# Optimization experiments

Measured on AMD Instinct MI355X. Metric: run time of the kernel, lower is better.

The kernel has to match this reference:

```python
import jax, jax.numpy as jnp
import numpy as np

N_HEAD = 16
HEAD_DIM = 64


def _shift(BD):
    # BD: [b, n, L, 2L] -> [b, n, L, L] (Transformer-XL left-shift trick)
    b, n, L, _ = BD.shape
    BD = jnp.pad(BD, ((0, 0), (0, 0), (0, 0), (0, 1)))          # [b,n,L,2L+1]
    BD = BD.reshape(b, n, 2 * L + 1, L)[:, :, :-1]              # [b,n,2L,L]
    BD = BD.reshape(b, n, L, 2 * L)[:, :, :, L:]                # [b,n,L,L]
    return BD


def _transpose_shift(E):
    # E: [b, n, L, 2L] -> [b, n, L, L]
    b, n, L, _ = E.shape
    E = jnp.pad(E, ((0, 0), (0, 0), (0, 0), (0, 1)))            # [b,n,L,2L+1]
    E = E.reshape(b, n, 2 * L + 1, L)                           # [b,n,2L+1,L]
    E = E[:, :, 1::2, :]                                        # rows 1,3,...,2L-1 -> [b,n,L,L]
    return E


def setup_inputs() -> dict:
    key = jax.random.key(0)
    ks = jax.random.split(key, 6)
    B, L, D = 4, 1024, 1024
    return {
        "x": jax.random.normal(ks[0], (B, L, D), jnp.float32),
        "pos_embed": jax.random.normal(ks[1], (2 * L, HEAD_DIM), jnp.float32),
        "W_qkv": jax.random.normal(ks[2], (D, 3 * D), jnp.float32) * (1.0 / np.sqrt(D)),
        "b_qkv": jax.random.normal(ks[3], (3 * D,), jnp.float32) * 0.01,
        "r_r_bias": jax.random.normal(ks[4], (N_HEAD, HEAD_DIM), jnp.float32) * 0.02,
        "r_w_bias": jax.random.normal(ks[5], (N_HEAD, HEAD_DIM), jnp.float32) * 0.02,
    }


def reference(x, pos_embed, W_qkv, b_qkv, r_r_bias, r_w_bias):
    b, L, d_model = x.shape
    scale = jnp.sqrt(jnp.asarray(HEAD_DIM, x.dtype))

    qkv = x @ W_qkv + b_qkv                                      # [b,L,3D]
    q, k, v = jnp.split(qkv, 3, axis=-1)

    def split_heads(t):  # [b,L,D] -> [b,n,L,hd]
        return t.reshape(b, L, N_HEAD, HEAD_DIM).transpose(0, 2, 1, 3)

    q, k, v = split_heads(q), split_heads(k), split_heads(v)

    rw_head_q = q + r_r_bias[None, :, None, :]
    AC = jnp.einsum('bnqd,bnkd->bnqk', rw_head_q, k)             # [b,n,L,L]
    D_ = jnp.einsum('nd,ld->nl', r_w_bias, pos_embed)[None, :, None, :]  # [1,n,1,2L]
    B_ = jnp.einsum('bnqd,ld->bnql', q, pos_embed)               # [b,n,L,2L]
    E_ = jnp.einsum('bnqd,ld->bnql', k, pos_embed)               # [b,n,L,2L]

    BDE = _shift(B_ + D_) + _transpose_shift(E_)
    attn = jax.nn.softmax((AC + BDE) / scale, axis=-1)

    out = jnp.einsum('bnqk,bnkd->bnqd', attn, v)                 # [b,n,L,hd]
    out = out.transpose(0, 2, 1, 3).reshape(b, L, d_model)       # merge heads
    return out
```

## Files before the change

### kernel.cpp

```cpp
#include <hip/hip_runtime.h>
#include <math.h>

typedef unsigned short u16;
typedef unsigned int u32;
typedef __attribute__((ext_vector_type(8))) short bf16x8;
typedef __attribute__((ext_vector_type(4))) float f32x4;

#define AS1 __attribute__((address_space(1)))
#define AS3 __attribute__((address_space(3)))

static __device__ __forceinline__ u16 f2b(float f) {
  u32 u = __float_as_uint(f);
  return (u16)((u + 0x7FFFu + ((u >> 16) & 1u)) >> 16);
}
static __device__ __forceinline__ float b2f(u16 b) {
  return __uint_as_float(((u32)b) << 16);
}

__global__ __launch_bounds__(256) void prep(
    const float* __restrict__ x, const float* __restrict__ W,
    const float* __restrict__ P,
    u16* __restrict__ xb, u16* __restrict__ Wt, u16* __restrict__ Pb)
{
  __shared__ u16 sT[64 * 68];
  const int bid = blockIdx.x, t = threadIdx.x;
  if (bid < 4096) {
    const size_t base = (size_t)bid * 1024 + t * 4;
    const float4 v = *(const float4*)(x + base);
    const u32 lo = (u32)f2b(v.x) | ((u32)f2b(v.y) << 16);
    const u32 hi = (u32)f2b(v.z) | ((u32)f2b(v.w) << 16);
    *(uint2*)(xb + base) = make_uint2(lo, hi);
  } else if (bid < 4224) {
    const size_t base = (size_t)(bid - 4096) * 1024 + t * 4;
    const float4 v = *(const float4*)(P + base);
    const u32 lo = (u32)f2b(v.x) | ((u32)f2b(v.y) << 16);
    const u32 hi = (u32)f2b(v.z) | ((u32)f2b(v.w) << 16);
    *(uint2*)(Pb + base) = make_uint2(lo, hi);
  } else if (bid < 4992) {
    const int tb = bid - 4224;
    const int tk = tb / 48, tn = tb % 48;
    const int k0 = tk * 64, n0 = tn * 64;
#pragma unroll
    for (int it = 0; it < 4; ++it) {
      const int c = it * 256 + t;
      const int r = c >> 4, c4 = (c & 15) << 2;
      const float4 v = *(const float4*)(W + (size_t)(k0 + r) * 3072 + n0 + c4);
      sT[(c4 + 0) * 68 + r] = f2b(v.x);
      sT[(c4 + 1) * 68 + r] = f2b(v.y);
      sT[(c4 + 2) * 68 + r] = f2b(v.z);
      sT[(c4 + 3) * 68 + r] = f2b(v.w);
    }
    __syncthreads();
#pragma unroll
    for (int it = 0; it < 4; ++it) {
      const int c = it * 256 + t;
      const int rr = c >> 4, k4 = (c & 15) << 2;
      const uint2 rv = *(const uint2*)(sT + rr * 68 + k4);
      *(uint2*)(Wt + (size_t)(n0 + rr) * 1024 + k0 + k4) = rv;
    }
  } else {
    if (t < 64) Pb[2048 * 64 + t] = f2b(P[2047 * 64 + t]);
  }
}

__global__ __launch_bounds__(256, 3) void qkv_gemm(
    const u16* __restrict__ xb, const u16* __restrict__ Wt,
    const float* __restrict__ bq,
    u16* __restrict__ Qh, u16* __restrict__ Kh, u16* __restrict__ Vt)
{
  __shared__ u16 smem[16384];
  u16* const sA = smem;
  u16* const sB = smem + 8192;
  u16* const T  = smem;
  const int t = threadIdx.x;
  const int lane = t & 63, w = t >> 6;
  const int l = lane & 15, ql = lane >> 4;
  const int wm = w & 1, wn = w >> 1;
  const int vid = blockIdx.x;
  const int xcd = vid & 7, jj = vid >> 3;
  const int n0 = (xcd * 3 + (jj % 3)) * 128;
  const int m0 = (jj / 3) * 128;

  f32x4 acc[4][4];
#pragma unroll
  for (int i = 0; i < 4; ++i)
#pragma unroll
    for (int j = 0; j < 4; ++j) acc[i][j] = (f32x4){0.f, 0.f, 0.f, 0.f};

  for (int k0 = 0; k0 < 1024; k0 += 64) {
    __syncthreads();
#pragma unroll
    for (int j = 0; j < 4; ++j) {
      const int ii = w * 4 + j;
      const int m = ii * 8 + (lane >> 3);
      const int q8 = (lane & 7) ^ (m & 7);
      __builtin_amdgcn_global_load_lds(
          (const AS1 u32*)(xb + (size_t)(m0 + m) * 1024 + k0 + q8 * 8),
          (AS3 u32*)(sA + ii * 512), 16, 0, 0);
      __builtin_amdgcn_global_load_lds(
          (const AS1 u32*)(Wt + (size_t)(n0 + m) * 1024 + k0 + q8 * 8),
          (AS3 u32*)(sB + ii * 512), 16, 0, 0);
    }
    __syncthreads();
#pragma unroll
    for (int ks = 0; ks < 2; ++ks) {
      bf16x8 a[4], b[4];
#pragma unroll
      for (int mt = 0; mt < 4; ++mt) {
        const int m = wm * 64 + mt * 16 + l;
        a[mt] = *(const bf16x8*)(sA + m * 64 + (((ks * 4 + ql) ^ (m & 7)) * 8));
      }
#pragma unroll
      for (int nt = 0; nt < 4; ++nt) {
        const int nn = wn * 64 + nt * 16 + l;
        b[nt] = *(const bf16x8*)(sB + nn * 64 + (((ks * 4 + ql) ^ (nn & 7)) * 8));
      }
#pragma unroll
      for (int mt = 0; mt < 4; ++mt)
#pragma unroll
        for (int nt = 0; nt < 4; ++nt)
          acc[mt][nt] = __builtin_amdgcn_mfma_f32_16x16x32_bf16(
              a[mt], b[nt], acc[mt][nt], 0, 0, 0);
    }
  }

  const int which = n0 >> 10;
  const int qbase = m0 & 1023;
  const int bb = m0 >> 10;
  const int h0 = (n0 & 1023) >> 6;
#pragma unroll
  for (int pass = 0; pass < 2; ++pass) {
    __syncthreads();
    if (wm == pass) {
#pragma unroll
      for (int nt = 0; nt < 4; ++nt) {
        const int col = wn * 64 + nt * 16 + l;
        const float bias = bq[n0 + col];
#pragma unroll
        for (int mt = 0; mt < 4; ++mt)
#pragma unroll
          for (int rg = 0; rg < 4; ++rg)
            T[(mt * 16 + ql * 4 + rg) * 136 + col] = f2b(acc[mt][nt][rg] + bias);
      }
    }
    __syncthreads();
    if (which < 2) {
      u16* const dst = which ? Kh : Qh;
#pragma unroll
      for (int h = 0; h < 2; ++h) {
        const size_t bnoff = ((size_t)(bb * 16 + h0 + h)) << 16;
#pragma unroll
        for (int it = 0; it < 2; ++it) {
          const int c = it * 256 + t;
          const int r = c >> 3, d8 = (c & 7) * 8;
          const uint4 v = *(const uint4*)(T + r * 136 + h * 64 + d8);
          *(uint4*)(dst + bnoff + ((size_t)(qbase + pass * 64 + r) << 6) + d8) = v;
        }
      }
    } else {
#pragma unroll
      for (int h = 0; h < 2; ++h) {
        const size_t bnoff = ((size_t)(bb * 16 + h0 + h)) << 16;
#pragma unroll
        for (int it = 0; it < 2; ++it) {
          const int c = it * 256 + t;
          const int dr = c >> 3, q8 = (c & 7) * 8;
          u32 pk[4];
#pragma unroll
          for (int e = 0; e < 4; ++e) {
            const u16 lo = T[(q8 + 2 * e + 0) * 136 + h * 64 + dr];
            const u16 hi = T[(q8 + 2 * e + 1) * 136 + h * 64 + dr];
            pk[e] = (u32)lo | ((u32)hi << 16);
          }
          *(uint4*)(Vt + bnoff + ((size_t)dr << 10) + qbase + pass * 64 + q8) =
              make_uint4(pk[0], pk[1], pk[2], pk[3]);
        }
      }
    }
  }
}

__global__ __launch_bounds__(256, 4) void rel_attn(
    const u16* __restrict__ Qh, const u16* __restrict__ Kh,
    const u16* __restrict__ Vt, const u16* __restrict__ Pb,
    const float* __restrict__ rrb, const float* __restrict__ rwb,
    float* __restrict__ out)
{
  __shared__ u16 smem[20480];
  u16* const sK    = smem;
  u16* const sVT   = smem + 4096;
  u16* const sProb = smem + 8192;
  u16* const sP    = smem + 12288;
  u16* const sU    = sP;
  u16* const sW    = sP + 4096;

  const int t = threadIdx.x;
  const int lane = t & 63, w = t >> 6;
  const int l = lane & 15, ql = lane >> 4;
  const int vid = blockIdx.x;
  const int bn = ((vid >> 7) << 3) | (vid & 7);
  const int qt = (vid >> 3) & 15;
  const int n = bn & 15, bb = bn >> 4;
  const size_t hoff = (size_t)bn << 16;
  const int cq = 3 - w;
  const int q0 = qt << 6;

#pragma unroll
  for (int it = 0; it < 2; ++it) {
    const int c = it * 256 + t;
    const int i = c >> 3, ch = c & 7;
    const int d8 = ch * 8;
    const uint4 qv = *(const uint4*)(Qh + hoff + ((size_t)(q0 + i) << 6) + d8);
    const uint4 kv = *(const uint4*)(Kh + hoff + ((size_t)(q0 + i) << 6) + d8);
    const u16* qp = (const u16*)&qv;
    const u16* kp = (const u16*)&kv;
    u16 uo[8], wo[8];
#pragma unroll
    for (int e = 0; e < 8; ++e) {
      const float rv = rrb[n * 64 + d8 + e];
      const float wv = rwb[n * 64 + d8 + e];
      const float qf = b2f(qp[e]), kf = b2f(kp[e]);
      uo[e] = f2b(qf + rv);
      wo[e] = f2b(qf + wv + kf);
    }
    const int pos = i * 64 + ((ch ^ (i & 7)) * 8);
    *(uint4*)(sU + pos) = *(const uint4*)uo;
    *(uint4*)(sW + pos) = *(const uint4*)wo;
  }
  __syncthreads();

  bf16x8 au[2], aw[2];
#pragma unroll
  for (int ks = 0; ks < 2; ++ks) {
    const int row = w * 16 + l;
    const int off = row * 64 + (((ks * 4 + ql) ^ (row & 7)) * 8);
    au[ks] = *(const bf16x8*)(sU + off);
    aw[ks] = *(const bf16x8*)(sW + off);
  }

  f32x4 o[4];
  float lrun[4];
#pragma unroll
  for (int ii = 0; ii < 4; ++ii) {
    o[ii] = (f32x4){0.f, 0.f, 0.f, 0.f};
    lrun[ii] = 0.f;
  }

  for (int k0 = 0; k0 < 1024; k0 += 64) {
    const int lb = 961 + k0 - q0;
    __syncthreads();
#pragma unroll
    for (int j = 0; j < 2; ++j) {
      const int ii = w * 2 + j;
      const int m = ii * 8 + (lane >> 3);
      const int q8 = (lane & 7) ^ (m & 7);
      __builtin_amdgcn_global_load_lds(
          (const AS1 u32*)(Kh + hoff + ((size_t)(k0 + m) << 6) + q8 * 8),
          (AS3 u32*)(sK + ii * 512), 16, 0, 0);
      __builtin_amdgcn_global_load_lds(
          (const AS1 u32*)(Vt + hoff + ((size_t)m << 10) + k0 + q8 * 8),
          (AS3 u32*)(sVT + ii * 512), 16, 0, 0);
    }
#pragma unroll
    for (int j = 0; j < 4; ++j) {
      const int ii = w * 4 + j;
      const int m = ii * 8 + (lane >> 3);
      const int q8 = (lane & 7) ^ (m & 7);
      __builtin_amdgcn_global_load_lds(
          (const AS1 u32*)(Pb + ((size_t)(lb + m) << 6) + q8 * 8),
          (AS3 u32*)(sP + ii * 512), 16, 0, 0);
    }
    __syncthreads();

    f32x4 z1[4], z2[5];
#pragma unroll
    for (int i = 0; i < 4; ++i) z1[i] = (f32x4){0.f, 0.f, 0.f, 0.f};
#pragma unroll
    for (int i = 0; i < 5; ++i) z2[i] = (f32x4){0.f, 0.f, 0.f, 0.f};
#pragma unroll
    for (int ks = 0; ks < 2; ++ks) {
#pragma unroll
      for (int nt = 0; nt < 4; ++nt) {
        const int row = nt * 16 + l;
        const bf16x8 bk =
            *(const bf16x8*)(sK + row * 64 + (((ks * 4 + ql) ^ (row & 7)) * 8));
        z1[nt] = __builtin_amdgcn_mfma_f32_16x16x32_bf16(au[ks], bk, z1[nt], 0, 0, 0);
      }
#pragma unroll
      for (int li2 = 0; li2 < 5; ++li2) {
        const int row = (li2 + cq) * 16 + l;
        const bf16x8 bp =
            *(const bf16x8*)(sP + row * 64 + (((ks * 4 + ql) ^ (row & 7)) * 8));
        z2[li2] = __builtin_amdgcn_mfma_f32_16x16x32_bf16(aw[ks], bp, z2[li2], 0, 0, 0);
      }
    }

    float p[4][4];
#pragma unroll
    for (int ii = 0; ii < 4; ++ii) {
      const int ci = 15 - ql * 4 - ii;
      const int src = (lane & 48) | ((l + ci) & 15);
      const bool wrap = l < ci;
#pragma unroll
      for (int jt = 0; jt < 4; ++jt) {
        const float val = wrap ? z2[jt + 1][ii] : z2[jt][ii];
        const float g = __shfl(val, src, 64);
        const float pv = exp2f((z1[jt][ii] + g) * 0.18033688011112042f);
        p[ii][jt] = pv;
        lrun[ii] += pv;
      }
    }

#pragma unroll
    for (int ii = 0; ii < 4; ++ii) {
      const int r = w * 16 + ql * 4 + ii;
#pragma unroll
      for (int jt = 0; jt < 4; ++jt) {
        const int ch = jt * 2 + (l >> 3);
        sProb[r * 64 + ((ch ^ (r & 7)) * 8) + (l & 7)] = f2b(p[ii][jt]);
      }
    }

#pragma unroll
    for (int ks = 0; ks < 2; ++ks) {
      const int ar = w * 16 + l;
      const bf16x8 ap =
          *(const bf16x8*)(sProb + ar * 64 + (((ks * 4 + ql) ^ (ar & 7)) * 8));
#pragma unroll
      for (int dt = 0; dt < 4; ++dt) {
        const int row = dt * 16 + l;
        const bf16x8 bv =
            *(const bf16x8*)(sVT + row * 64 + (((ks * 4 + ql) ^ (row & 7)) * 8));
        o[dt] = __builtin_amdgcn_mfma_f32_16x16x32_bf16(ap, bv, o[dt], 0, 0, 0);
      }
    }
  }

#pragma unroll
  for (int ii = 0; ii < 4; ++ii) {
    float ls = lrun[ii];
    ls += __shfl_xor(ls, 1);
    ls += __shfl_xor(ls, 2);
    ls += __shfl_xor(ls, 4);
    ls += __shfl_xor(ls, 8);
    const float inv = 1.f / ls;
    const int q = q0 + w * 16 + ql * 4 + ii;
#pragma unroll
    for (int dt = 0; dt < 4; ++dt)
      out[((size_t)(bb * 1024 + q) << 10) + (n << 6) + dt * 16 + l] =
          o[dt][ii] * inv;
  }
}

extern "C" void kernel_launch(void* const* d_in, const int* in_sizes, int n_in,
                              void* d_out, int out_size, void* d_ws, size_t ws_size,
                              hipStream_t stream) {
  const float* x  = (const float*)d_in[0];
  const float* P  = (const float*)d_in[1];
  const float* Wq = (const float*)d_in[2];
  const float* bq = (const float*)d_in[3];
  const float* rr = (const float*)d_in[4];
  const float* rw = (const float*)d_in[5];
  float* out = (float*)d_out;

  char* ws = (char*)d_ws;
  u16* xb = (u16*)(ws);
  u16* Wt = (u16*)(ws + 8388608);
  u16* Pb = (u16*)(ws + 14680064);
  u16* Qh = (u16*)(ws + 14946304);
  u16* Kh = (u16*)(ws + 23334912);
  u16* Vt = (u16*)(ws + 31723520);

  prep<<<4993, 256, 0, stream>>>(x, Wq, P, xb, Wt, Pb);
  qkv_gemm<<<768, 256, 0, stream>>>(xb, Wt, bq, Qh, Kh, Vt);
  rel_attn<<<1024, 256, 0, stream>>>(Qh, Kh, Vt, Pb, rr, rw, out);
}
```

Measured before the change: 184.5 us.

## Double query tile per block in rel_attn to reuse K, V and pos tiles

```diff
diff --git a/kernel.cpp b/kernel.cpp
--- a/kernel.cpp
+++ b/kernel.cpp
@@ -12,6 +12,9 @@
 static __device__ __forceinline__ u16 f2b(float f) {
   u32 u = __float_as_uint(f);
   return (u16)((u + 0x7FFFu + ((u >> 16) & 1u)) >> 16);
+}
+static __device__ __forceinline__ u16 f2b_fast(float f) {
+  return (u16)((__float_as_uint(f) + 0x8000u) >> 16);
 }
 static __device__ __forceinline__ float b2f(u16 b) {
   return __uint_as_float(((u32)b) << 16);
@@ -180,33 +183,32 @@
   }
 }
 
-__global__ __launch_bounds__(256, 4) void rel_attn(
+__global__ __launch_bounds__(256, 2) void rel_attn(
     const u16* __restrict__ Qh, const u16* __restrict__ Kh,
     const u16* __restrict__ Vt, const u16* __restrict__ Pb,
     const float* __restrict__ rrb, const float* __restrict__ rwb,
     float* __restrict__ out)
 {
-  __shared__ u16 smem[20480];
+  __shared__ u16 smem[24576];
   u16* const sK    = smem;
   u16* const sVT   = smem + 4096;
   u16* const sProb = smem + 8192;
   u16* const sP    = smem + 12288;
-  u16* const sU    = sP;
-  u16* const sW    = sP + 4096;
+  u16* const sU    = smem;
+  u16* const sW    = smem + 8192;
 
   const int t = threadIdx.x;
   const int lane = t & 63, w = t >> 6;
   const int l = lane & 15, ql = lane >> 4;
   const int vid = blockIdx.x;
-  const int bn = ((vid >> 7) << 3) | (vid & 7);
-  const int qt = (vid >> 3) & 15;
+  const int qt = vid >> 6, bn = vid & 63;
   const int n = bn & 15, bb = bn >> 4;
   const size_t hoff = (size_t)bn << 16;
-  const int cq = 3 - w;
-  const int q0 = qt << 6;
-
-#pragma unroll
-  for (int it = 0; it < 2; ++it) {
+  const int q0 = qt << 7;
+  const int bz = 6 - 2 * w;
+
+#pragma unroll
+  for (int it = 0; it < 4; ++it) {
     const int c = it * 256 + t;
     const int i = c >> 3, ch = c & 7;
     const int d8 = ch * 8;
@@ -229,25 +231,29 @@
   }
   __syncthreads();
 
-  bf16x8 au[2], aw[2];
-#pragma unroll
-  for (int ks = 0; ks < 2; ++ks) {
-    const int row = w * 16 + l;
-    const int off = row * 64 + (((ks * 4 + ql) ^ (row & 7)) * 8);
-    au[ks] = *(const bf16x8*)(sU + off);
-    aw[ks] = *(const bf16x8*)(sW + off);
-  }
-
-  f32x4 o[4];
-  float lrun[4];
-#pragma unroll
-  for (int ii = 0; ii < 4; ++ii) {
-    o[ii] = (f32x4){0.f, 0.f, 0.f, 0.f};
-    lrun[ii] = 0.f;
-  }
+  bf16x8 au[2][2], aw[2][2];
+#pragma unroll
+  for (int mt = 0; mt < 2; ++mt)
+#pragma unroll
+    for (int ks = 0; ks < 2; ++ks) {
+      const int row = w * 32 + mt * 16 + l;
+      const int off = row * 64 + (((ks * 4 + ql) ^ (row & 7)) * 8);
+      au[mt][ks] = *(const bf16x8*)(sU + off);
+      aw[mt][ks] = *(const bf16x8*)(sW + off);
+    }
+
+  f32x4 o[2][4];
+  float lrun[2][4];
+#pragma unroll
+  for (int mt = 0; mt < 2; ++mt)
+#pragma unroll
+    for (int ii = 0; ii < 4; ++ii) {
+      o[mt][ii] = (f32x4){0.f, 0.f, 0.f, 0.f};
+      lrun[mt][ii] = 0.f;
+    }
 
   for (int k0 = 0; k0 < 1024; k0 += 64) {
-    const int lb = 961 + k0 - q0;
+    const int lbase = 897 + k0 - q0;
     __syncthreads();
 #pragma unroll
     for (int j = 0; j < 2; ++j) {
@@ -262,21 +268,24 @@
           (AS3 u32*)(sVT + ii * 512), 16, 0, 0);
     }
 #pragma unroll
-    for (int j = 0; j < 4; ++j) {
-      const int ii = w * 4 + j;
+    for (int j = 0; j < 6; ++j) {
+      const int ii = w * 6 + j;
       const int m = ii * 8 + (lane >> 3);
       const int q8 = (lane & 7) ^ (m & 7);
       __builtin_amdgcn_global_load_lds(
-          (const AS1 u32*)(Pb + ((size_t)(lb + m) << 6) + q8 * 8),
+          (const AS1 u32*)(Pb + ((size_t)(lbase + m) << 6) + q8 * 8),
           (AS3 u32*)(sP + ii * 512), 16, 0, 0);
     }
     __syncthreads();
 
-    f32x4 z1[4], z2[5];
-#pragma unroll
-    for (int i = 0; i < 4; ++i) z1[i] = (f32x4){0.f, 0.f, 0.f, 0.f};
-#pragma unroll
-    for (int i = 0; i < 5; ++i) z2[i] = (f32x4){0.f, 0.f, 0.f, 0.f};
+    f32x4 z1[2][4], z2[2][5];
+#pragma unroll
+    for (int mt = 0; mt < 2; ++mt) {
+#pragma unroll
+      for (int i = 0; i < 4; ++i) z1[mt][i] = (f32x4){0.f, 0.f, 0.f, 0.f};
+#pragma unroll
+      for (int i = 0; i < 5; ++i) z2[mt][i] = (f32x4){0.f, 0.f, 0.f, 0.f};
+    }
 #pragma unroll
     for (int ks = 0; ks < 2; ++ks) {
 #pragma unroll
@@ -284,72 +293,94 @@
         const int row = nt * 16 + l;
         const bf16x8 bk =
             *(const bf16x8*)(sK + row * 64 + (((ks * 4 + ql) ^ (row & 7)) * 8));
-        z1[nt] = __builtin_amdgcn_mfma_f32_16x16x32_bf16(au[ks], bk, z1[nt], 0, 0, 0);
-      }
-#pragma unroll
-      for (int li2 = 0; li2 < 5; ++li2) {
-        const int row = (li2 + cq) * 16 + l;
+#pragma unroll
+        for (int mt = 0; mt < 2; ++mt)
+          z1[mt][nt] = __builtin_amdgcn_mfma_f32_16x16x32_bf16(
+              au[mt][ks], bk, z1[mt][nt], 0, 0, 0);
+      }
+#pragma unroll
+      for (int rt = 0; rt < 6; ++rt) {
+        const int row = (bz + rt) * 16 + l;
         const bf16x8 bp =
             *(const bf16x8*)(sP + row * 64 + (((ks * 4 + ql) ^ (row & 7)) * 8));
-        z2[li2] = __builtin_amdgcn_mfma_f32_16x16x32_bf16(aw[ks], bp, z2[li2], 0, 0, 0);
-      }
-    }
-
-    float p[4][4];
-#pragma unroll
-    for (int ii = 0; ii < 4; ++ii) {
-      const int ci = 15 - ql * 4 - ii;
-      const int src = (lane & 48) | ((l + ci) & 15);
-      const bool wrap = l < ci;
-#pragma unroll
-      for (int jt = 0; jt < 4; ++jt) {
-        const float val = wrap ? z2[jt + 1][ii] : z2[jt][ii];
-        const float g = __shfl(val, src, 64);
-        const float pv = exp2f((z1[jt][ii] + g) * 0.18033688011112042f);
-        p[ii][jt] = pv;
-        lrun[ii] += pv;
-      }
-    }
-
-#pragma unroll
-    for (int ii = 0; ii < 4; ++ii) {
-      const int r = w * 16 + ql * 4 + ii;
-#pragma unroll
-      for (int jt = 0; jt < 4; ++jt) {
-        const int ch = jt * 2 + (l >> 3);
-        sProb[r * 64 + ((ch ^ (r & 7)) * 8) + (l & 7)] = f2b(p[ii][jt]);
-      }
-    }
+        if (rt >= 1)
+          z2[0][rt - 1] = __builtin_amdgcn_mfma_f32_16x16x32_bf16(
+              aw[0][ks], bp, z2[0][rt - 1], 0, 0, 0);
+        if (rt <= 4)
+          z2[1][rt] = __builtin_amdgcn_mfma_f32_16x16x32_bf16(
+              aw[1][ks], bp, z2[1][rt], 0, 0, 0);
+      }
+    }
+
+    float p[2][4][4];
+#pragma unroll
+    for (int mt = 0; mt < 2; ++mt)
+#pragma unroll
+      for (int ii = 0; ii < 4; ++ii) {
+        const int ci = 15 - ql * 4 - ii;
+        const int src = (lane & 48) | ((l + ci) & 15);
+        const bool wrap = l < ci;
+#pragma unroll
+        for (int jt = 0; jt < 4; ++jt) {
+          const float val = wrap ? z2[mt][jt + 1][ii] : z2[mt][jt][ii];
+          const float g = __shfl(val, src, 64);
+          const float pv = exp2f((z1[mt][jt][ii] + g) * 0.18033688011112042f);
+          p[mt][ii][jt] = pv;
+          lrun[mt][ii] += pv;
+        }
+      }
 
 #pragma unroll
     for (int ks = 0; ks < 2; ++ks) {
-      const int ar = w * 16 + l;
-      const bf16x8 ap =
-          *(const bf16x8*)(sProb + ar * 64 + (((ks * 4 + ql) ^ (ar & 7)) * 8));
+#pragma unroll
+      for (int mt = 0; mt < 2; ++mt)
+#pragma unroll
+        for (int ii = 0; ii < 4; ++ii) {
+          const int r = w * 32 + mt * 16 + ql * 4 + ii;
+          const int sw2 = (r & 3) ^ ((r >> 2) & 3);
+#pragma unroll
+          for (int jh = 0; jh < 2; ++jh) {
+            const int ch = jh * 2 + (l >> 3);
+            sProb[r * 32 + ((ch ^ sw2) * 8) + (l & 7)] =
+                f2b_fast(p[mt][ii][ks * 2 + jh]);
+          }
+        }
+      bf16x8 bv[4];
 #pragma unroll
       for (int dt = 0; dt < 4; ++dt) {
         const int row = dt * 16 + l;
-        const bf16x8 bv =
+        bv[dt] =
             *(const bf16x8*)(sVT + row * 64 + (((ks * 4 + ql) ^ (row & 7)) * 8));
-        o[dt] = __builtin_amdgcn_mfma_f32_16x16x32_bf16(ap, bv, o[dt], 0, 0, 0);
+      }
+#pragma unroll
+      for (int mt = 0; mt < 2; ++mt) {
+        const int ar = w * 32 + mt * 16 + l;
+        const bf16x8 ap = *(const bf16x8*)(
+            sProb + ar * 32 + ((ql ^ ((ar & 3) ^ ((ar >> 2) & 3))) * 8));
+#pragma unroll
+        for (int dt = 0; dt < 4; ++dt)
+          o[mt][dt] = __builtin_amdgcn_mfma_f32_16x16x32_bf16(
+              ap, bv[dt], o[mt][dt], 0, 0, 0);
       }
     }
   }
 
 #pragma unroll
-  for (int ii = 0; ii < 4; ++ii) {
-    float ls = lrun[ii];
-    ls += __shfl_xor(ls, 1);
-    ls += __shfl_xor(ls, 2);
-    ls += __shfl_xor(ls, 4);
-    ls += __shfl_xor(ls, 8);
-    const float inv = 1.f / ls;
-    const int q = q0 + w * 16 + ql * 4 + ii;
-#pragma unroll
-    for (int dt = 0; dt < 4; ++dt)
-      out[((size_t)(bb * 1024 + q) << 10) + (n << 6) + dt * 16 + l] =
-          o[dt][ii] * inv;
-  }
+  for (int mt = 0; mt < 2; ++mt)
+#pragma unroll
+    for (int ii = 0; ii < 4; ++ii) {
+      float ls = lrun[mt][ii];
+      ls += __shfl_xor(ls, 1);
+      ls += __shfl_xor(ls, 2);
+      ls += __shfl_xor(ls, 4);
+      ls += __shfl_xor(ls, 8);
+      const float inv = 1.f / ls;
+      const int q = q0 + w * 32 + mt * 16 + ql * 4 + ii;
+#pragma unroll
+      for (int dt = 0; dt < 4; ++dt)
+        out[((size_t)(bb * 1024 + q) << 10) + (n << 6) + dt * 16 + l] =
+            o[mt][dt][ii] * inv;
+    }
 }
 
 extern "C" void kernel_launch(void* const* d_in, const int* in_sizes, int n_in,
@@ -373,5 +404,5 @@
 
   prep<<<4993, 256, 0, stream>>>(x, Wq, P, xb, Wt, Pb);
   qkv_gemm<<<768, 256, 0, stream>>>(xb, Wt, bq, Qh, Kh, Vt);
-  rel_attn<<<1024, 256, 0, stream>>>(Qh, Kh, Vt, Pb, rr, rw, out);
-}
+  rel_attn<<<512, 256, 0, stream>>>(Qh, Kh, Vt, Pb, rr, rw, out);
+}
```

Result: faster. 175.5 us (-4.9%).

## Double-buffer K/V tiles and ring-buffer positional tiles to overlap loads with compute

Applied to the files above, without the earlier changes.

```diff
diff --git a/kernel.cpp b/kernel.cpp
--- a/kernel.cpp
+++ b/kernel.cpp
@@ -12,6 +12,9 @@
 static __device__ __forceinline__ u16 f2b(float f) {
   u32 u = __float_as_uint(f);
   return (u16)((u + 0x7FFFu + ((u >> 16) & 1u)) >> 16);
+}
+static __device__ __forceinline__ u16 f2b_fast(float f) {
+  return (u16)((__float_as_uint(f) + 0x8000u) >> 16);
 }
 static __device__ __forceinline__ float b2f(u16 b) {
   return __uint_as_float(((u32)b) << 16);
@@ -180,19 +183,18 @@
   }
 }
 
-__global__ __launch_bounds__(256, 4) void rel_attn(
+__global__ __launch_bounds__(256, 2) void rel_attn(
     const u16* __restrict__ Qh, const u16* __restrict__ Kh,
     const u16* __restrict__ Vt, const u16* __restrict__ Pb,
     const float* __restrict__ rrb, const float* __restrict__ rwb,
     float* __restrict__ out)
 {
-  __shared__ u16 smem[20480];
-  u16* const sK    = smem;
-  u16* const sVT   = smem + 4096;
-  u16* const sProb = smem + 8192;
-  u16* const sP    = smem + 12288;
-  u16* const sU    = sP;
-  u16* const sW    = sP + 4096;
+  __shared__ u16 smem[30720];
+  u16* const sVT0  = smem + 8192;
+  u16* const sP0   = smem;
+  u16* const sProb = smem + 28672;
+  u16* const sU    = smem;
+  u16* const sW    = smem + 4096;
 
   const int t = threadIdx.x;
   const int lane = t & 63, w = t >> 6;
@@ -204,6 +206,7 @@
   const size_t hoff = (size_t)bn << 16;
   const int cq = 3 - w;
   const int q0 = qt << 6;
+  const int pbase = 961 - q0;
 
 #pragma unroll
   for (int it = 0; it < 2; ++it) {
@@ -237,41 +240,63 @@
     au[ks] = *(const bf16x8*)(sU + off);
     aw[ks] = *(const bf16x8*)(sW + off);
   }
-
-  f32x4 o[4];
-  float lrun[4];
-#pragma unroll
-  for (int ii = 0; ii < 4; ++ii) {
-    o[ii] = (f32x4){0.f, 0.f, 0.f, 0.f};
-    lrun[ii] = 0.f;
-  }
-
-  for (int k0 = 0; k0 < 1024; k0 += 64) {
-    const int lb = 961 + k0 - q0;
-    __syncthreads();
+  __syncthreads();
+
+  {
 #pragma unroll
     for (int j = 0; j < 2; ++j) {
       const int ii = w * 2 + j;
       const int m = ii * 8 + (lane >> 3);
       const int q8 = (lane & 7) ^ (m & 7);
       __builtin_amdgcn_global_load_lds(
-          (const AS1 u32*)(Kh + hoff + ((size_t)(k0 + m) << 6) + q8 * 8),
-          (AS3 u32*)(sK + ii * 512), 16, 0, 0);
-      __builtin_amdgcn_global_load_lds(
-          (const AS1 u32*)(Vt + hoff + ((size_t)m << 10) + k0 + q8 * 8),
-          (AS3 u32*)(sVT + ii * 512), 16, 0, 0);
-    }
-#pragma unroll
-    for (int j = 0; j < 4; ++j) {
-      const int ii = w * 4 + j;
-      const int m = ii * 8 + (lane >> 3);
-      const int q8 = (lane & 7) ^ (m & 7);
-      __builtin_amdgcn_global_load_lds(
-          (const AS1 u32*)(Pb + ((size_t)(lb + m) << 6) + q8 * 8),
-          (AS3 u32*)(sP + ii * 512), 16, 0, 0);
-    }
-    __syncthreads();
-
+          (const AS1 u32*)(Kh + hoff + ((size_t)m << 6) + q8 * 8),
+          (AS3 u32*)(smem + ii * 512), 16, 0, 0);
+      __builtin_amdgcn_global_load_lds(
+          (const AS1 u32*)(Vt + hoff + ((size_t)m << 10) + q8 * 8),
+          (AS3 u32*)(smem + 8192 + ii * 512), 16, 0, 0);
+      __builtin_amdgcn_global_load_lds(
+          (const AS1 u32*)(Pb + ((size_t)(pbase + m) << 6) + q8 * 8),
+          (AS3 u32*)(smem + 16384 + ii * 512), 16, 0, 0);
+      __builtin_amdgcn_global_load_lds(
+          (const AS1 u32*)(Pb + ((size_t)(pbase + 64 + m) << 6) + q8 * 8),
+          (AS3 u32*)(smem + 20480 + ii * 512), 16, 0, 0);
+    }
+  }
+
+  f32x4 o[4];
+  float lrun[4];
+#pragma unroll
+  for (int ii = 0; ii < 4; ++ii) {
+    o[ii] = (f32x4){0.f, 0.f, 0.f, 0.f};
+    lrun[ii] = 0.f;
+  }
+
+  int c0 = 16384, c1 = 20480, c2 = 24576;
+
+  for (int tt = 0; tt < 16; ++tt) {
+    __syncthreads();
+    if (tt < 15) {
+      const int kn = (tt + 1) << 6;
+      const int kb_n = ((tt + 1) & 1) * 4096;
+      const int prow = pbase + ((tt + 2) << 6);
+#pragma unroll
+      for (int j = 0; j < 2; ++j) {
+        const int ii = w * 2 + j;
+        const int m = ii * 8 + (lane >> 3);
+        const int q8 = (lane & 7) ^ (m & 7);
+        __builtin_amdgcn_global_load_lds(
+            (const AS1 u32*)(Kh + hoff + ((size_t)(kn + m) << 6) + q8 * 8),
+            (AS3 u32*)(smem + kb_n + ii * 512), 16, 0, 0);
+        __builtin_amdgcn_global_load_lds(
+            (const AS1 u32*)(Vt + hoff + ((size_t)m << 10) + kn + q8 * 8),
+            (AS3 u32*)(smem + 8192 + kb_n + ii * 512), 16, 0, 0);
+        __builtin_amdgcn_global_load_lds(
+            (const AS1 u32*)(Pb + ((size_t)(prow + m) << 6) + q8 * 8),
+            (AS3 u32*)(smem + c2 + ii * 512), 16, 0, 0);
+      }
+    }
+
+    const int kb = (tt & 1) * 4096;
     f32x4 z1[4], z2[5];
 #pragma unroll
     for (int i = 0; i < 4; ++i) z1[i] = (f32x4){0.f, 0.f, 0.f, 0.f};
@@ -282,15 +307,17 @@
 #pragma unroll
       for (int nt = 0; nt < 4; ++nt) {
         const int row = nt * 16 + l;
-        const bf16x8 bk =
-            *(const bf16x8*)(sK + row * 64 + (((ks * 4 + ql) ^ (row & 7)) * 8));
+        const bf16x8 bk = *(const bf16x8*)(
+            smem + kb + row * 64 + (((ks * 4 + ql) ^ (row & 7)) * 8));
         z1[nt] = __builtin_amdgcn_mfma_f32_16x16x32_bf16(au[ks], bk, z1[nt], 0, 0, 0);
       }
 #pragma unroll
       for (int li2 = 0; li2 < 5; ++li2) {
-        const int row = (li2 + cq) * 16 + l;
-        const bf16x8 bp =
-            *(const bf16x8*)(sP + row * 64 + (((ks * 4 + ql) ^ (row & 7)) * 8));
+        const int T = li2 + cq;
+        const int base = (T >= 4) ? c1 : c0;
+        const int rw2 = (T & 3) * 16 + l;
+        const bf16x8 bp = *(const bf16x8*)(
+            smem + base + rw2 * 64 + (((ks * 4 + ql) ^ (rw2 & 7)) * 8));
         z2[li2] = __builtin_amdgcn_mfma_f32_16x16x32_bf16(aw[ks], bp, z2[li2], 0, 0, 0);
       }
     }
@@ -312,28 +339,31 @@
     }
 
 #pragma unroll
-    for (int ii = 0; ii < 4; ++ii) {
-      const int r = w * 16 + ql * 4 + ii;
-#pragma unroll
-      for (int jt = 0; jt < 4; ++jt) {
-        const int ch = jt * 2 + (l >> 3);
-        sProb[r * 64 + ((ch ^ (r & 7)) * 8) + (l & 7)] = f2b(p[ii][jt]);
-      }
-    }
-
-#pragma unroll
     for (int ks = 0; ks < 2; ++ks) {
+#pragma unroll
+      for (int ii = 0; ii < 4; ++ii) {
+        const int r = w * 16 + ql * 4 + ii;
+        const int sw2 = (r & 3) ^ ((r >> 2) & 3);
+#pragma unroll
+        for (int jh = 0; jh < 2; ++jh) {
+          const int ch = jh * 2 + (l >> 3);
+          sProb[r * 32 + ((ch ^ sw2) * 8) + (l & 7)] =
+              f2b_fast(p[ii][ks * 2 + jh]);
+        }
+      }
       const int ar = w * 16 + l;
-      const bf16x8 ap =
-          *(const bf16x8*)(sProb + ar * 64 + (((ks * 4 + ql) ^ (ar & 7)) * 8));
+      const bf16x8 ap = *(const bf16x8*)(
+          sProb + ar * 32 + ((ql ^ ((ar & 3) ^ ((ar >> 2) & 3))) * 8));
 #pragma unroll
       for (int dt = 0; dt < 4; ++dt) {
         const int row = dt * 16 + l;
-        const bf16x8 bv =
-            *(const bf16x8*)(sVT + row * 64 + (((ks * 4 + ql) ^ (row & 7)) * 8));
+        const bf16x8 bv = *(const bf16x8*)(
+            smem + 8192 + kb + row * 64 + (((ks * 4 + ql) ^ (row & 7)) * 8));
         o[dt] = __builtin_amdgcn_mfma_f32_16x16x32_bf16(ap, bv, o[dt], 0, 0, 0);
       }
     }
+
+    const int tmp = c0; c0 = c1; c1 = c2; c2 = tmp;
   }
 
 #pragma unroll
```

After: 179.6 us. 1.03x faster.

## Process 128-key tiles per iteration in rel_attn with larger LDS staging

Applied to the files above, without the earlier changes.

```diff
diff --git a/kernel.cpp b/kernel.cpp
--- a/kernel.cpp
+++ b/kernel.cpp
@@ -12,6 +12,9 @@
 static __device__ __forceinline__ u16 f2b(float f) {
   u32 u = __float_as_uint(f);
   return (u16)((u + 0x7FFFu + ((u >> 16) & 1u)) >> 16);
+}
+static __device__ __forceinline__ u16 f2b_fast(float f) {
+  return (u16)((__float_as_uint(f) + 0x8000u) >> 16);
 }
 static __device__ __forceinline__ float b2f(u16 b) {
   return __uint_as_float(((u32)b) << 16);
@@ -180,19 +183,16 @@
   }
 }
 
-__global__ __launch_bounds__(256, 4) void rel_attn(
+__global__ __launch_bounds__(256, 2) void rel_attn(
     const u16* __restrict__ Qh, const u16* __restrict__ Kh,
     const u16* __restrict__ Vt, const u16* __restrict__ Pb,
     const float* __restrict__ rrb, const float* __restrict__ rwb,
     float* __restrict__ out)
 {
-  __shared__ u16 smem[20480];
-  u16* const sK    = smem;
-  u16* const sVT   = smem + 4096;
-  u16* const sProb = smem + 8192;
-  u16* const sP    = smem + 12288;
-  u16* const sU    = sP;
-  u16* const sW    = sP + 4096;
+  __shared__ u16 smem[32768];
+  u16* const sProb = smem + 28672;
+  u16* const sU    = smem;
+  u16* const sW    = smem + 4096;
 
   const int t = threadIdx.x;
   const int lane = t & 63, w = t >> 6;
@@ -239,106 +239,122 @@
   }
 
   f32x4 o[4];
-  float lrun[4];
+  f32x4 lr[4];
 #pragma unroll
   for (int ii = 0; ii < 4; ++ii) {
     o[ii] = (f32x4){0.f, 0.f, 0.f, 0.f};
-    lrun[ii] = 0.f;
-  }
-
-  for (int k0 = 0; k0 < 1024; k0 += 64) {
+    lr[ii] = (f32x4){0.f, 0.f, 0.f, 0.f};
+  }
+
+  for (int tt = 0; tt < 8; ++tt) {
+    const int k0 = tt << 7;
     const int lb = 961 + k0 - q0;
     __syncthreads();
-#pragma unroll
-    for (int j = 0; j < 2; ++j) {
-      const int ii = w * 2 + j;
-      const int m = ii * 8 + (lane >> 3);
-      const int q8 = (lane & 7) ^ (m & 7);
-      __builtin_amdgcn_global_load_lds(
-          (const AS1 u32*)(Kh + hoff + ((size_t)(k0 + m) << 6) + q8 * 8),
-          (AS3 u32*)(sK + ii * 512), 16, 0, 0);
-      __builtin_amdgcn_global_load_lds(
-          (const AS1 u32*)(Vt + hoff + ((size_t)m << 10) + k0 + q8 * 8),
-          (AS3 u32*)(sVT + ii * 512), 16, 0, 0);
-    }
 #pragma unroll
     for (int j = 0; j < 4; ++j) {
       const int ii = w * 4 + j;
       const int m = ii * 8 + (lane >> 3);
       const int q8 = (lane & 7) ^ (m & 7);
       __builtin_amdgcn_global_load_lds(
+          (const AS1 u32*)(Kh + hoff + ((size_t)(k0 + m) << 6) + q8 * 8),
+          (AS3 u32*)(smem + ii * 512), 16, 0, 0);
+      const int h = ii >> 3, ii2 = ii & 7;
+      const int d = ii2 * 8 + (lane >> 3);
+      const int q8v = (lane & 7) ^ (d & 7);
+      __builtin_amdgcn_global_load_lds(
+          (const AS1 u32*)(Vt + hoff + ((size_t)d << 10) + k0 + h * 64 + q8v * 8),
+          (AS3 u32*)(smem + 8192 + h * 4096 + ii2 * 512), 16, 0, 0);
+    }
+#pragma unroll
+    for (int j = 0; j < 6; ++j) {
+      const int ii = w * 6 + j;
+      const int m = ii * 8 + (lane >> 3);
+      const int q8 = (lane & 7) ^ (m & 7);
+      __builtin_amdgcn_global_load_lds(
           (const AS1 u32*)(Pb + ((size_t)(lb + m) << 6) + q8 * 8),
-          (AS3 u32*)(sP + ii * 512), 16, 0, 0);
-    }
-    __syncthreads();
-
-    f32x4 z1[4], z2[5];
-#pragma unroll
-    for (int i = 0; i < 4; ++i) z1[i] = (f32x4){0.f, 0.f, 0.f, 0.f};
-#pragma unroll
-    for (int i = 0; i < 5; ++i) z2[i] = (f32x4){0.f, 0.f, 0.f, 0.f};
+          (AS3 u32*)(smem + 16384 + ii * 512), 16, 0, 0);
+    }
+    __syncthreads();
+
+    f32x4 z1[2][4], z2[2][5];
+#pragma unroll
+    for (int s = 0; s < 2; ++s) {
+#pragma unroll
+      for (int i = 0; i < 4; ++i) z1[s][i] = (f32x4){0.f, 0.f, 0.f, 0.f};
+#pragma unroll
+      for (int i = 0; i < 5; ++i) z2[s][i] = (f32x4){0.f, 0.f, 0.f, 0.f};
+    }
 #pragma unroll
     for (int ks = 0; ks < 2; ++ks) {
 #pragma unroll
-      for (int nt = 0; nt < 4; ++nt) {
-        const int row = nt * 16 + l;
-        const bf16x8 bk =
-            *(const bf16x8*)(sK + row * 64 + (((ks * 4 + ql) ^ (row & 7)) * 8));
-        z1[nt] = __builtin_amdgcn_mfma_f32_16x16x32_bf16(au[ks], bk, z1[nt], 0, 0, 0);
-      }
-#pragma unroll
-      for (int li2 = 0; li2 < 5; ++li2) {
-        const int row = (li2 + cq) * 16 + l;
-        const bf16x8 bp =
-            *(const bf16x8*)(sP + row * 64 + (((ks * 4 + ql) ^ (row & 7)) * 8));
-        z2[li2] = __builtin_amdgcn_mfma_f32_16x16x32_bf16(aw[ks], bp, z2[li2], 0, 0, 0);
-      }
-    }
-
-    float p[4][4];
+      for (int s = 0; s < 2; ++s) {
+#pragma unroll
+        for (int nt = 0; nt < 4; ++nt) {
+          const int row = s * 64 + nt * 16 + l;
+          const bf16x8 bk = *(const bf16x8*)(
+              smem + row * 64 + (((ks * 4 + ql) ^ (row & 7)) * 8));
+          z1[s][nt] = __builtin_amdgcn_mfma_f32_16x16x32_bf16(
+              au[ks], bk, z1[s][nt], 0, 0, 0);
+        }
+#pragma unroll
+        for (int li2 = 0; li2 < 5; ++li2) {
+          const int row = s * 64 + (li2 + cq) * 16 + l;
+          const bf16x8 bp = *(const bf16x8*)(
+              smem + 16384 + row * 64 + (((ks * 4 + ql) ^ (row & 7)) * 8));
+          z2[s][li2] = __builtin_amdgcn_mfma_f32_16x16x32_bf16(
+              aw[ks], bp, z2[s][li2], 0, 0, 0);
+        }
+      }
+    }
+
+    float p[2][4][4];
 #pragma unroll
     for (int ii = 0; ii < 4; ++ii) {
       const int ci = 15 - ql * 4 - ii;
       const int src = (lane & 48) | ((l + ci) & 15);
       const bool wrap = l < ci;
 #pragma unroll
-      for (int jt = 0; jt < 4; ++jt) {
-        const float val = wrap ? z2[jt + 1][ii] : z2[jt][ii];
-        const float g = __shfl(val, src, 64);
-        const float pv = exp2f((z1[jt][ii] + g) * 0.18033688011112042f);
-        p[ii][jt] = pv;
-        lrun[ii] += pv;
-      }
-    }
-
-#pragma unroll
-    for (int ii = 0; ii < 4; ++ii) {
-      const int r = w * 16 + ql * 4 + ii;
-#pragma unroll
-      for (int jt = 0; jt < 4; ++jt) {
-        const int ch = jt * 2 + (l >> 3);
-        sProb[r * 64 + ((ch ^ (r & 7)) * 8) + (l & 7)] = f2b(p[ii][jt]);
-      }
-    }
-
-#pragma unroll
-    for (int ks = 0; ks < 2; ++ks) {
-      const int ar = w * 16 + l;
-      const bf16x8 ap =
-          *(const bf16x8*)(sProb + ar * 64 + (((ks * 4 + ql) ^ (ar & 7)) * 8));
-#pragma unroll
-      for (int dt = 0; dt < 4; ++dt) {
-        const int row = dt * 16 + l;
-        const bf16x8 bv =
-            *(const bf16x8*)(sVT + row * 64 + (((ks * 4 + ql) ^ (row & 7)) * 8));
-        o[dt] = __builtin_amdgcn_mfma_f32_16x16x32_bf16(ap, bv, o[dt], 0, 0, 0);
+      for (int s = 0; s < 2; ++s)
+#pragma unroll
+        for (int jt = 0; jt < 4; ++jt) {
+          const float val = wrap ? z2[s][jt + 1][ii] : z2[s][jt][ii];
+          const float g = __shfl(val, src, 64);
+          const float pv = exp2f((z1[s][jt][ii] + g) * 0.18033688011112042f);
+          p[s][ii][jt] = pv;
+          lr[ii][jt] += pv;
+        }
+    }
+
+#pragma unroll
+    for (int s = 0; s < 2; ++s) {
+#pragma unroll
+      for (int ii = 0; ii < 4; ++ii) {
+        const int r = w * 16 + ql * 4 + ii;
+#pragma unroll
+        for (int jt = 0; jt < 4; ++jt) {
+          const int ch = jt * 2 + (l >> 3);
+          sProb[r * 64 + ((ch ^ (r & 7)) * 8) + (l & 7)] = f2b_fast(p[s][ii][jt]);
+        }
+      }
+#pragma unroll
+      for (int ks = 0; ks < 2; ++ks) {
+        const int ar = w * 16 + l;
+        const bf16x8 ap = *(const bf16x8*)(
+            sProb + ar * 64 + (((ks * 4 + ql) ^ (ar & 7)) * 8));
+#pragma unroll
+        for (int dt = 0; dt < 4; ++dt) {
+          const int row = dt * 16 + l;
+          const bf16x8 bv = *(const bf16x8*)(
+              smem + 8192 + s * 4096 + row * 64 + (((ks * 4 + ql) ^ (row & 7)) * 8));
+          o[dt] = __builtin_amdgcn_mfma_f32_16x16x32_bf16(ap, bv, o[dt], 0, 0, 0);
+        }
       }
     }
   }
 
 #pragma unroll
   for (int ii = 0; ii < 4; ++ii) {
-    float ls = lrun[ii];
+    float ls = lr[ii][0] + lr[ii][1] + lr[ii][2] + lr[ii][3];
     ls += __shfl_xor(ls, 1);
     ls += __shfl_xor(ls, 2);
     ls += __shfl_xor(ls, 4);
```

After: 188.4 us. +2.1%, slower.
